# Optimization experiments

Hardware: AMD Instinct MI355X
Metric: run time of the kernel (lower is better)

Reference implementation:

```python
import jax, jax.numpy as jnp
import numpy as np

N, E = 50000, 800000
D_IN, D_HID, D_OUT, K = 128, 64, 64, 3
SLOPE = 0.2


def _xavier(key, shape):
    fan_out, fan_in = shape[0], shape[-1]
    if len(shape) == 3:  # att param (1, heads, 2*out)
        fan_out, fan_in = shape[1], shape[2]
    a = jnp.sqrt(6.0 / (fan_in + fan_out)).astype(jnp.float32)
    return jax.random.uniform(key, shape, jnp.float32, -a, a)


def setup_inputs() -> dict:
    key = jax.random.key(0)
    ks = jax.random.split(key, 9)
    x = jax.random.normal(ks[0], (N, D_IN), jnp.float32)
    edge_index = jax.random.randint(ks[1], (2, E), 0, N, jnp.int64)
    return {
        "x": x,
        "edge_index": edge_index,
        "W1": _xavier(ks[2], (D_HID, D_IN)),        # lin weight layer 1
        "att1": _xavier(ks[3], (1, 1, 2 * D_HID)),
        "bias1": jnp.zeros((D_HID,), jnp.float32),
        "resW1": _xavier(ks[4], (D_HID, D_IN)),     # res_fc (128 != 64)
        "W2": _xavier(ks[5], (D_OUT, D_HID)),       # lin weight layer 2
        "att2": _xavier(ks[6], (1, 1, 2 * D_OUT)),
        "bias2": jnp.zeros((D_OUT,), jnp.float32),
    }


def _agdn_conv(x, src, dst, W, att, bias, resW, heads):
    n = x.shape[0]
    h0 = (x @ W.T).reshape(n, heads, -1)                      # [N, h, out]
    feats = [h0]
    f = h0
    for _ in range(K):  # K-hop scatter-add propagation
        f = jax.ops.segment_sum(f[src], dst, num_segments=n)  # [N, h, out]
        feats.append(f)
    stack = jnp.stack(feats, axis=2)                          # [N, h, K+1, out]
    cat = jnp.concatenate(
        [jnp.broadcast_to(h0[:, :, None, :], stack.shape), stack], axis=-1
    )                                                         # [N, h, K+1, 2*out]
    score = jax.nn.leaky_relu((cat * att).sum(-1), SLOPE)     # [N, h, K+1]
    attn = jax.nn.softmax(score, axis=2)[..., None]
    out = (stack * attn).sum(axis=2).reshape(n, -1)           # [N, h*out]
    res = (x @ resW.T) if resW is not None else h0.reshape(n, -1)
    return out + res + bias


def reference(x, edge_index, W1, att1, bias1, resW1, W2, att2, bias2):
    src, dst = edge_index[0], edge_index[1]
    h = _agdn_conv(x, src, dst, W1, att1, bias1, resW1, heads=1)
    h = jax.nn.elu(h)  # eval mode: dropout is identity
    out = _agdn_conv(h, src, dst, W2, att2, bias2, None, heads=1)
    return out
```

## Files before the change

kernel.cpp:

```cpp
#include <hip/hip_runtime.h>
#include <math.h>


#define EPB 4096
#define CAP 8192

typedef __attribute__((ext_vector_type(8))) short bf16x8;
typedef __attribute__((ext_vector_type(4))) float f32x4;
typedef __attribute__((ext_vector_type(2))) float f32x2;

__device__ __forceinline__ unsigned short f2bf(float f)
{
    unsigned int t = __builtin_bit_cast(unsigned int, f);
    t += 0x7FFFu + ((t >> 16) & 1u);
    return (unsigned short)(t >> 16);
}
__device__ __forceinline__ float bflo(unsigned int u)
{
    return __builtin_bit_cast(float, u << 16);
}
__device__ __forceinline__ float bfhi(unsigned int u)
{
    return __builtin_bit_cast(float, u & 0xFFFF0000u);
}
__device__ __forceinline__ f32x2 up2v(unsigned int u)
{
    f32x2 r;
    r.x = bflo(u);
    r.y = bfhi(u);
    return r;
}

#define LD1 136
__global__ __launch_bounds__(256)
void gemm_l1_mfma(const float* __restrict__ x,
                  const unsigned short* __restrict__ w1b,
                  unsigned short* __restrict__ h0, float* __restrict__ res, int n)
{
    __shared__ unsigned short xs[64 * LD1];
    __shared__ unsigned short ws[128 * LD1];
    const int tid = threadIdx.x;
    const int n0 = blockIdx.x * 64;

    for (int i = tid; i < 128 * 16; i += 256) {
        int r = i >> 4, c8 = (i & 15) * 8;
        *(uint4*)&ws[r * LD1 + c8] = *(const uint4*)&w1b[r * 128 + c8];
    }
    for (int i = tid; i < 64 * 32; i += 256) {
        int r = i >> 5, c4 = (i & 31) * 4;
        int nn = n0 + r;
        float4 v = (nn < n) ? *(const float4*)&x[(size_t)nn * 128 + c4]
                            : make_float4(0.f, 0.f, 0.f, 0.f);
        uint2 o;
        o.x = (unsigned)f2bf(v.x) | ((unsigned)f2bf(v.y) << 16);
        o.y = (unsigned)f2bf(v.z) | ((unsigned)f2bf(v.w) << 16);
        *(uint2*)&xs[r * LD1 + c4] = o;
    }
    __syncthreads();

    const int wv = tid >> 6, l = tid & 63;
    const int lrow = l & 15, lk = l >> 4;
    f32x4 acc[8] = {};
    const unsigned short* ax = &xs[(wv * 16 + lrow) * LD1 + lk * 8];
    const unsigned short* bw = &ws[lrow * LD1 + lk * 8];

    #pragma unroll
    for (int s = 0; s < 4; ++s) {
        bf16x8 a = *(const bf16x8*)&ax[s * 32];
        #pragma unroll
        for (int t = 0; t < 8; ++t) {
            bf16x8 b = *(const bf16x8*)&bw[(size_t)t * 16 * LD1 + s * 32];
            acc[t] = __builtin_amdgcn_mfma_f32_16x16x32_bf16(a, b, acc[t], 0, 0, 0);
        }
    }

    #pragma unroll
    for (int t = 0; t < 8; ++t) {
        #pragma unroll
        for (int r = 0; r < 4; ++r) {
            int node = n0 + wv * 16 + lk * 4 + r;
            if (node < n) {
                if (t < 4) h0[(size_t)node * 64 + t * 16 + lrow] = f2bf(acc[t][r]);
                else       res[(size_t)node * 64 + (t - 4) * 16 + lrow] = acc[t][r];
            }
        }
    }
}

#define LD2 72
__global__ __launch_bounds__(256)
void gemm_l2_mfma(const float* __restrict__ h,
                  const unsigned short* __restrict__ w2b,
                  unsigned short* __restrict__ h0, int n)
{
    __shared__ unsigned short xs[64 * LD2];
    __shared__ unsigned short ws[64 * LD2];
    const int tid = threadIdx.x;
    const int n0 = blockIdx.x * 64;

    for (int i = tid; i < 64 * 8; i += 256) {
        int r = i >> 3, c8 = (i & 7) * 8;
        *(uint4*)&ws[r * LD2 + c8] = *(const uint4*)&w2b[r * 64 + c8];
    }
    for (int i = tid; i < 64 * 16; i += 256) {
        int r = i >> 4, c4 = (i & 15) * 4;
        int nn = n0 + r;
        float4 v = (nn < n) ? *(const float4*)&h[(size_t)nn * 64 + c4]
                            : make_float4(0.f, 0.f, 0.f, 0.f);
        uint2 o;
        o.x = (unsigned)f2bf(v.x) | ((unsigned)f2bf(v.y) << 16);
        o.y = (unsigned)f2bf(v.z) | ((unsigned)f2bf(v.w) << 16);
        *(uint2*)&xs[r * LD2 + c4] = o;
    }
    __syncthreads();

    const int wv = tid >> 6, l = tid & 63;
    const int lrow = l & 15, lk = l >> 4;
    f32x4 acc[4] = {};
    const unsigned short* ax = &xs[(wv * 16 + lrow) * LD2 + lk * 8];
    const unsigned short* bw = &ws[lrow * LD2 + lk * 8];

    #pragma unroll
    for (int s = 0; s < 2; ++s) {
        bf16x8 a = *(const bf16x8*)&ax[s * 32];
        #pragma unroll
        for (int t = 0; t < 4; ++t) {
            bf16x8 b = *(const bf16x8*)&bw[(size_t)t * 16 * LD2 + s * 32];
            acc[t] = __builtin_amdgcn_mfma_f32_16x16x32_bf16(a, b, acc[t], 0, 0, 0);
        }
    }

    #pragma unroll
    for (int t = 0; t < 4; ++t) {
        #pragma unroll
        for (int r = 0; r < 4; ++r) {
            int node = n0 + wv * 16 + lk * 4 + r;
            if (node < n)
                h0[(size_t)node * 64 + t * 16 + lrow] = f2bf(acc[t][r]);
        }
    }
}

__global__ __launch_bounds__(256)
void part_hist_kernel(const int* __restrict__ dst, int* __restrict__ table,
                      int E, int NB,
                      const float* __restrict__ W1, const float* __restrict__ Wres,
                      const float* __restrict__ W2,
                      unsigned short* __restrict__ w1b, unsigned short* __restrict__ w2b)
{
    int gi = blockIdx.x * 256 + threadIdx.x;
    if (gi < 8192)       w1b[gi] = f2bf(W1[gi]);
    else if (gi < 16384) w1b[gi] = f2bf(Wres[gi - 8192]);
    else if (gi < 20480) w2b[gi - 16384] = f2bf(W2[gi - 16384]);

    __shared__ int h[256];
    h[threadIdx.x] = 0;
    __syncthreads();
    int base = blockIdx.x * EPB;
    for (int i = threadIdx.x; i < EPB; i += 256) {
        int e = base + i;
        if (e < E) atomicAdd(&h[((unsigned)dst[e]) >> 8], 1);
    }
    __syncthreads();
    table[threadIdx.x * NB + blockIdx.x] = h[threadIdx.x];
}

__global__ __launch_bounds__(256)
void scanA_kernel(const int* __restrict__ cnt, int* __restrict__ excl,
                  int* __restrict__ bsum, int n)
{
    __shared__ int sh[256];
    int i = blockIdx.x * 256 + threadIdx.x;
    int v = (i < n) ? cnt[i] : 0;
    sh[threadIdx.x] = v;
    __syncthreads();
    #pragma unroll
    for (int off = 1; off < 256; off <<= 1) {
        int t = (threadIdx.x >= off) ? sh[threadIdx.x - off] : 0;
        __syncthreads();
        sh[threadIdx.x] += t;
        __syncthreads();
    }
    if (i < n) excl[i] = sh[threadIdx.x] - v;
    if (threadIdx.x == 255) bsum[blockIdx.x] = sh[255];
}

__global__ __launch_bounds__(256)
void part_scatter_kernel(const int* __restrict__ src, const int* __restrict__ dst,
                         const int* __restrict__ exclT, const int* __restrict__ bsumT,
                         unsigned int* __restrict__ packed, int E, int NB, int nbT)
{
    __shared__ int lhist[256];
    __shared__ int sh[256];
    __shared__ int lexcl[256];
    __shared__ int lcur[256];
    __shared__ int gb2[256];
    __shared__ int bofsL[256];
    __shared__ unsigned int lp[EPB];
    __shared__ unsigned char lbin[EPB];

    const int tid = threadIdx.x;
    const int base = blockIdx.x * EPB;
    const int cntE = min(EPB, E - base);

    unsigned int pv[16];
    int pb[16];
    lhist[tid] = 0;
    __syncthreads();
    #pragma unroll
    for (int it = 0; it < 16; ++it) {
        int i = it * 256 + tid;
        pv[it] = 0; pb[it] = -1;
        if (i < cntE) {
            int e = base + i;
            unsigned int p = (((unsigned)dst[e]) << 16) | (unsigned)src[e];
            pv[it] = p;
            pb[it] = (int)(p >> 24);
            atomicAdd(&lhist[pb[it]], 1);
        }
    }
    __syncthreads();
    sh[tid] = lhist[tid];
    __syncthreads();
    #pragma unroll
    for (int off = 1; off < 256; off <<= 1) {
        int t = (tid >= off) ? sh[tid - off] : 0;
        __syncthreads();
        sh[tid] += t;
        __syncthreads();
    }
    lexcl[tid] = sh[tid] - lhist[tid];
    lcur[tid] = sh[tid] - lhist[tid];
    __syncthreads();
    int bv = (tid < nbT) ? bsumT[tid] : 0;
    sh[tid] = bv;
    __syncthreads();
    #pragma unroll
    for (int off = 1; off < 256; off <<= 1) {
        int t = (tid >= off) ? sh[tid - off] : 0;
        __syncthreads();
        sh[tid] += t;
        __syncthreads();
    }
    bofsL[tid] = sh[tid] - bv;
    __syncthreads();
    int ti = tid * NB + blockIdx.x;
    gb2[tid] = exclT[ti] + bofsL[ti >> 8] - lexcl[tid];
    __syncthreads();
    #pragma unroll
    for (int it = 0; it < 16; ++it) {
        if (pb[it] >= 0) {
            int slot = atomicAdd(&lcur[pb[it]], 1);
            lp[slot] = pv[it];
            lbin[slot] = (unsigned char)pb[it];
        }
    }
    __syncthreads();
    for (int i = tid; i < cntE; i += 256)
        packed[gb2[lbin[i]] + i] = lp[i];
}

__global__ __launch_bounds__(256)
void bucket_build_kernel(const unsigned int* __restrict__ packed,
                         const int* __restrict__ exclT, const int* __restrict__ bsumT,
                         int* __restrict__ rowptr, int* __restrict__ col,
                         int E, int NB, int N, int nbT)
{
    __shared__ int h[256];
    __shared__ int sh[256];
    __shared__ int lcur[256];
    __shared__ int bofsL[256];
    __shared__ unsigned int lp[CAP];
    __shared__ unsigned short colS[CAP];

    const int b = blockIdx.x;
    const int t = threadIdx.x;

    int bv = (t < nbT) ? bsumT[t] : 0;
    sh[t] = bv;
    __syncthreads();
    #pragma unroll
    for (int off = 1; off < 256; off <<= 1) {
        int v = (t >= off) ? sh[t - off] : 0;
        __syncthreads();
        sh[t] += v;
        __syncthreads();
    }
    bofsL[t] = sh[t] - bv;
    __syncthreads();

    int i0 = exclT[b * NB] + bofsL[(b * NB) >> 8];
    int bn = (b + 1) * NB;
    int i1 = (b == gridDim.x - 1) ? E : (exclT[bn] + bofsL[bn >> 8]);
    int cB = i1 - i0;

    h[t] = 0;
    __syncthreads();
    for (int i = t; i < cB; i += 256) {
        unsigned int p = packed[i0 + i];
        if (i < CAP) lp[i] = p;
        atomicAdd(&h[(p >> 16) & 255], 1);
    }
    __syncthreads();
    sh[t] = h[t];
    __syncthreads();
    #pragma unroll
    for (int off = 1; off < 256; off <<= 1) {
        int v = (t >= off) ? sh[t - off] : 0;
        __syncthreads();
        sh[t] += v;
        __syncthreads();
    }
    int excl = sh[t] - h[t];
    int d = b * 256 + t;
    if (d < N) rowptr[d] = i0 + excl;
    if (b == gridDim.x - 1 && t == 0) rowptr[N] = E;
    lcur[t] = excl;
    __syncthreads();
    for (int i = t; i < cB; i += 256) {
        unsigned int p = (i < CAP) ? lp[i] : packed[i0 + i];
        int lo = (p >> 16) & 255;
        int r = atomicAdd(&lcur[lo], 1);
        if (r < CAP) colS[r] = (unsigned short)(p & 0xFFFFu);
        else col[i0 + r] = (int)(p & 0xFFFFu);
    }
    __syncthreads();
    for (int i = t; i < cB && i < CAP; i += 256)
        col[i0 + i] = (int)colS[i];
}

__global__ __launch_bounds__(256)
void hop_csr_kernel(const unsigned short* __restrict__ fin,
                    unsigned short* __restrict__ fout,
                    const int* __restrict__ rowptr, const int* __restrict__ col, int n)
{
    int lane = threadIdx.x & 63;
    int node = blockIdx.x * 8 + ((threadIdx.x >> 6) << 1) + (lane >> 5);
    if (node >= n) return;
    int sub = (lane >> 3) & 3;
    int fo = (lane & 7) * 8;

    int beg = rowptr[node], end = rowptr[node + 1];
    f32x2 ac[4] = {};
    for (int b = beg + sub; b < end; b += 16) {
        int e1 = b + 4, e2 = b + 8, e3 = b + 12;
        uint4 u0 = *(const uint4*)&fin[(size_t)col[b] * 64 + fo];
        uint4 u1 = make_uint4(0, 0, 0, 0);
        uint4 u2 = make_uint4(0, 0, 0, 0);
        uint4 u3 = make_uint4(0, 0, 0, 0);
        if (e1 < end) u1 = *(const uint4*)&fin[(size_t)col[e1] * 64 + fo];
        if (e2 < end) u2 = *(const uint4*)&fin[(size_t)col[e2] * 64 + fo];
        if (e3 < end) u3 = *(const uint4*)&fin[(size_t)col[e3] * 64 + fo];
        ac[0] += up2v(u0.x); ac[1] += up2v(u0.y);
        ac[2] += up2v(u0.z); ac[3] += up2v(u0.w);
        ac[0] += up2v(u1.x); ac[1] += up2v(u1.y);
        ac[2] += up2v(u1.z); ac[3] += up2v(u1.w);
        ac[0] += up2v(u2.x); ac[1] += up2v(u2.y);
        ac[2] += up2v(u2.z); ac[3] += up2v(u2.w);
        ac[0] += up2v(u3.x); ac[1] += up2v(u3.y);
        ac[2] += up2v(u3.z); ac[3] += up2v(u3.w);
    }
    float a[8] = {ac[0].x, ac[0].y, ac[1].x, ac[1].y,
                  ac[2].x, ac[2].y, ac[3].x, ac[3].y};
    #pragma unroll
    for (int off = 8; off <= 16; off <<= 1)
        #pragma unroll
        for (int k = 0; k < 8; ++k)
            a[k] += __shfl_xor(a[k], off);
    if (sub == 0) {
        uint4 o;
        o.x = (unsigned)f2bf(a[0]) | ((unsigned)f2bf(a[1]) << 16);
        o.y = (unsigned)f2bf(a[2]) | ((unsigned)f2bf(a[3]) << 16);
        o.z = (unsigned)f2bf(a[4]) | ((unsigned)f2bf(a[5]) << 16);
        o.w = (unsigned)f2bf(a[6]) | ((unsigned)f2bf(a[7]) << 16);
        *(uint4*)&fout[(size_t)node * 64 + fo] = o;
    }
}

template<int MODE>
__global__ __launch_bounds__(256)
void hop3_combine_kernel(const unsigned short* __restrict__ h0,
                         const unsigned short* __restrict__ f1,
                         const unsigned short* __restrict__ f2,
                         const float* __restrict__ res, const float* __restrict__ att,
                         const float* __restrict__ bias, float* __restrict__ out,
                         const int* __restrict__ rowptr, const int* __restrict__ col, int n)
{
    int lane = threadIdx.x & 63;
    int node = blockIdx.x * 8 + ((threadIdx.x >> 6) << 1) + (lane >> 5);
    if (node >= n) return;
    int sub = (lane >> 3) & 3;
    int fo = (lane & 7) * 8;
    size_t rbase = (size_t)node * 64 + fo;

    int beg = rowptr[node], end = rowptr[node + 1];
    f32x2 ac[4] = {};
    for (int b = beg + sub; b < end; b += 16) {
        int e1 = b + 4, e2 = b + 8, e3 = b + 12;
        uint4 u0 = *(const uint4*)&f2[(size_t)col[b] * 64 + fo];
        uint4 u1 = make_uint4(0, 0, 0, 0);
        uint4 u2 = make_uint4(0, 0, 0, 0);
        uint4 u3 = make_uint4(0, 0, 0, 0);
        if (e1 < end) u1 = *(const uint4*)&f2[(size_t)col[e1] * 64 + fo];
        if (e2 < end) u2 = *(const uint4*)&f2[(size_t)col[e2] * 64 + fo];
        if (e3 < end) u3 = *(const uint4*)&f2[(size_t)col[e3] * 64 + fo];
        ac[0] += up2v(u0.x); ac[1] += up2v(u0.y);
        ac[2] += up2v(u0.z); ac[3] += up2v(u0.w);
        ac[0] += up2v(u1.x); ac[1] += up2v(u1.y);
        ac[2] += up2v(u1.z); ac[3] += up2v(u1.w);
        ac[0] += up2v(u2.x); ac[1] += up2v(u2.y);
        ac[2] += up2v(u2.z); ac[3] += up2v(u2.w);
        ac[0] += up2v(u3.x); ac[1] += up2v(u3.y);
        ac[2] += up2v(u3.z); ac[3] += up2v(u3.w);
    }
    float a[8] = {ac[0].x, ac[0].y, ac[1].x, ac[1].y,
                  ac[2].x, ac[2].y, ac[3].x, ac[3].y};
    #pragma unroll
    for (int off = 8; off <= 16; off <<= 1)
        #pragma unroll
        for (int k = 0; k < 8; ++k)
            a[k] += __shfl_xor(a[k], off);

    uint4 r0 = *(const uint4*)&h0[rbase];
    uint4 r1 = *(const uint4*)&f1[rbase];
    uint4 r2 = *(const uint4*)&f2[rbase];
    float v0f[8] = {bflo(r0.x), bfhi(r0.x), bflo(r0.y), bfhi(r0.y),
                    bflo(r0.z), bfhi(r0.z), bflo(r0.w), bfhi(r0.w)};
    float v1f[8] = {bflo(r1.x), bfhi(r1.x), bflo(r1.y), bfhi(r1.y),
                    bflo(r1.z), bfhi(r1.z), bflo(r1.w), bfhi(r1.w)};
    float v2f[8] = {bflo(r2.x), bfhi(r2.x), bflo(r2.y), bfhi(r2.y),
                    bflo(r2.z), bfhi(r2.z), bflo(r2.w), bfhi(r2.w)};

    float4 alo0 = *(const float4*)&att[fo];
    float4 alo1 = *(const float4*)&att[fo + 4];
    float4 ahi0 = *(const float4*)&att[64 + fo];
    float4 ahi1 = *(const float4*)&att[64 + fo + 4];
    float alo[8] = {alo0.x, alo0.y, alo0.z, alo0.w, alo1.x, alo1.y, alo1.z, alo1.w};
    float ahi[8] = {ahi0.x, ahi0.y, ahi0.z, ahi0.w, ahi1.x, ahi1.y, ahi1.z, ahi1.w};

    float p0 = 0.f, q0 = 0.f, q1 = 0.f, q2 = 0.f, q3 = 0.f;
    #pragma unroll
    for (int j = 0; j < 8; ++j) {
        p0 += v0f[j] * alo[j];
        q0 += v0f[j] * ahi[j];
        q1 += v1f[j] * ahi[j];
        q2 += v2f[j] * ahi[j];
        q3 += a[j]   * ahi[j];
    }
    #pragma unroll
    for (int off = 1; off <= 4; off <<= 1) {
        p0 += __shfl_xor(p0, off);
        q0 += __shfl_xor(q0, off);
        q1 += __shfl_xor(q1, off);
        q2 += __shfl_xor(q2, off);
        q3 += __shfl_xor(q3, off);
    }

    float s0 = p0 + q0, s1 = p0 + q1, s2 = p0 + q2, s3 = p0 + q3;
    s0 = s0 > 0.f ? s0 : 0.2f * s0;
    s1 = s1 > 0.f ? s1 : 0.2f * s1;
    s2 = s2 > 0.f ? s2 : 0.2f * s2;
    s3 = s3 > 0.f ? s3 : 0.2f * s3;
    float m = fmaxf(fmaxf(s0, s1), fmaxf(s2, s3));
    float E0 = __expf(s0 - m), E1 = __expf(s1 - m);
    float E2 = __expf(s2 - m), E3 = __expf(s3 - m);
    float inv = 1.f / (E0 + E1 + E2 + E3);
    float w0 = E0 * inv, w1 = E1 * inv, w2 = E2 * inv, w3 = E3 * inv;

    float rsv[8];
    if (MODE == 0) {
        float4 ra = *(const float4*)&res[rbase];
        float4 rb = *(const float4*)&res[rbase + 4];
        rsv[0] = ra.x; rsv[1] = ra.y; rsv[2] = ra.z; rsv[3] = ra.w;
        rsv[4] = rb.x; rsv[5] = rb.y; rsv[6] = rb.z; rsv[7] = rb.w;
    } else {
        #pragma unroll
        for (int j = 0; j < 8; ++j) rsv[j] = v0f[j];
    }
    float4 ba = *(const float4*)&bias[fo];
    float4 bb = *(const float4*)&bias[fo + 4];
    float bi[8] = {ba.x, ba.y, ba.z, ba.w, bb.x, bb.y, bb.z, bb.w};

    float o[8];
    #pragma unroll
    for (int j = 0; j < 8; ++j) {
        float v = w0 * v0f[j] + w1 * v1f[j] + w2 * v2f[j] + w3 * a[j];
        v += rsv[j] + bi[j];
        if (MODE == 0) v = v > 0.f ? v : __expf(v) - 1.f;
        o[j] = v;
    }
    if (sub == 0) {
        *(float4*)&out[rbase]     = make_float4(o[0], o[1], o[2], o[3]);
        *(float4*)&out[rbase + 4] = make_float4(o[4], o[5], o[6], o[7]);
    }
}

extern "C" void kernel_launch(void* const* d_in, const int* in_sizes, int n_in,
                              void* d_out, int out_size, void* d_ws, size_t ws_size,
                              hipStream_t stream)
{
    const float* x     = (const float*)d_in[0];
    const int*   ei    = (const int*)  d_in[1];
    const float* W1    = (const float*)d_in[2];
    const float* att1  = (const float*)d_in[3];
    const float* bias1 = (const float*)d_in[4];
    const float* resW1 = (const float*)d_in[5];
    const float* W2    = (const float*)d_in[6];
    const float* att2  = (const float*)d_in[7];
    const float* bias2 = (const float*)d_in[8];

    const int N_ = in_sizes[0] / 128;
    const int E_ = in_sizes[1] / 2;
    const int* src = ei;
    const int* dst = ei + E_;

    float* out = (float*)d_out;
    size_t S = (size_t)N_ * 64;
    unsigned short* h0 = (unsigned short*)d_ws;
    unsigned short* f1 = h0 + S;
    unsigned short* f2 = f1 + S;
    int* rowptr = (int*)(f2 + S);
    int* col    = rowptr + (N_ + 1);

    const int NB    = (E_ + EPB - 1) / EPB;
    const int NBUCK = (N_ + 255) / 256;

    unsigned int* packed = (unsigned int*)f1;
    int* table = (int*)(col + E_);
    int* exclT = table + 256 * NB;
    int* bsumT = exclT + 256 * NB;
    unsigned short* w1b = (unsigned short*)(bsumT + 256);
    unsigned short* w2b = w1b + 16384;

    dim3 blk(256);
    int grid_g    = (N_ + 63) / 64;
    int node_grid = (N_ + 7) / 8;
    int nT        = 256 * NB;
    int nbT       = (nT + 255) / 256;

    part_hist_kernel<<<NB, blk, 0, stream>>>(dst, table, E_, NB,
                                             W1, resW1, W2, w1b, w2b);
    scanA_kernel<<<nbT, blk, 0, stream>>>(table, exclT, bsumT, nT);
    part_scatter_kernel<<<NB, blk, 0, stream>>>(src, dst, exclT, bsumT, packed,
                                                E_, NB, nbT);
    bucket_build_kernel<<<NBUCK, blk, 0, stream>>>(packed, exclT, bsumT, rowptr, col,
                                                   E_, NB, N_, nbT);

    gemm_l1_mfma<<<grid_g, blk, 0, stream>>>(x, w1b, h0, out, N_);
    hop_csr_kernel<<<node_grid, blk, 0, stream>>>(h0, f1, rowptr, col, N_);
    hop_csr_kernel<<<node_grid, blk, 0, stream>>>(f1, f2, rowptr, col, N_);
    hop3_combine_kernel<0><<<node_grid, blk, 0, stream>>>(h0, f1, f2, out, att1, bias1, out,
                                                          rowptr, col, N_);

    gemm_l2_mfma<<<grid_g, blk, 0, stream>>>(out, w2b, h0, N_);
    hop_csr_kernel<<<node_grid, blk, 0, stream>>>(h0, f1, rowptr, col, N_);
    hop_csr_kernel<<<node_grid, blk, 0, stream>>>(f1, f2, rowptr, col, N_);
    hop3_combine_kernel<1><<<node_grid, blk, 0, stream>>>(h0, f1, f2, nullptr, att2, bias2, out,
                                                          rowptr, col, N_);
}
```

Before: 177.4 us.

## Fuse layer-1 GEMM with edge histogram kernel and drop bin byte array

The edge-partition histogram and the layer-1 MFMA GEMM now run as one launch, with the first NB blocks doing histogram work and the rest doing the GEMM. Each GEMM block converts W1/Wres from fp32 to bf16 itself instead of reading a prepacked buffer. This removes one kernel launch and lets the two independent stages overlap on the GPU. The scatter kernel also drops its lbin shared array and recomputes the bin from the packed word's top byte. In exchange, every GEMM block repeats the weight conversion.

```diff
diff --git a/kernel.cpp b/kernel.cpp
--- a/kernel.cpp
+++ b/kernel.cpp
@@ -33,18 +33,46 @@
 
 #define LD1 136
 __global__ __launch_bounds__(256)
-void gemm_l1_mfma(const float* __restrict__ x,
-                  const unsigned short* __restrict__ w1b,
-                  unsigned short* __restrict__ h0, float* __restrict__ res, int n)
+void gemm_l1_hist_kernel(const float* __restrict__ x,
+                         const float* __restrict__ W1, const float* __restrict__ Wres,
+                         unsigned short* __restrict__ h0, float* __restrict__ res, int n,
+                         const int* __restrict__ dst, int* __restrict__ table,
+                         int E, int NB,
+                         const float* __restrict__ W2, unsigned short* __restrict__ w2b)
 {
     __shared__ unsigned short xs[64 * LD1];
     __shared__ unsigned short ws[128 * LD1];
     const int tid = threadIdx.x;
-    const int n0 = blockIdx.x * 64;
-
-    for (int i = tid; i < 128 * 16; i += 256) {
-        int r = i >> 4, c8 = (i & 15) * 8;
-        *(uint4*)&ws[r * LD1 + c8] = *(const uint4*)&w1b[r * 128 + c8];
+
+    if ((int)blockIdx.x < NB) {
+        int hb = blockIdx.x;
+        int gi = hb * 256 + tid;
+        if (gi < 4096) w2b[gi] = f2bf(W2[gi]);
+
+        int* h = (int*)xs;
+        h[tid] = 0;
+        __syncthreads();
+        int base = hb * EPB;
+        for (int i = tid; i < EPB; i += 256) {
+            int e = base + i;
+            if (e < E) atomicAdd(&h[((unsigned)dst[e]) >> 8], 1);
+        }
+        __syncthreads();
+        table[tid * NB + hb] = h[tid];
+        return;
+    }
+
+    const int n0 = ((int)blockIdx.x - NB) * 64;
+
+    for (int i = tid; i < 128 * 32; i += 256) {
+        int r = i >> 5, c4 = (i & 31) * 4;
+        const float* wsrc = (r < 64) ? &W1[(size_t)r * 128 + c4]
+                                     : &Wres[(size_t)(r - 64) * 128 + c4];
+        float4 v = *(const float4*)wsrc;
+        uint2 o;
+        o.x = (unsigned)f2bf(v.x) | ((unsigned)f2bf(v.y) << 16);
+        o.y = (unsigned)f2bf(v.z) | ((unsigned)f2bf(v.w) << 16);
+        *(uint2*)&ws[r * LD1 + c4] = o;
     }
     for (int i = tid; i < 64 * 32; i += 256) {
         int r = i >> 5, c4 = (i & 31) * 4;
@@ -142,30 +170,6 @@
 }
 
 __global__ __launch_bounds__(256)
-void part_hist_kernel(const int* __restrict__ dst, int* __restrict__ table,
-                      int E, int NB,
-                      const float* __restrict__ W1, const float* __restrict__ Wres,
-                      const float* __restrict__ W2,
-                      unsigned short* __restrict__ w1b, unsigned short* __restrict__ w2b)
-{
-    int gi = blockIdx.x * 256 + threadIdx.x;
-    if (gi < 8192)       w1b[gi] = f2bf(W1[gi]);
-    else if (gi < 16384) w1b[gi] = f2bf(Wres[gi - 8192]);
-    else if (gi < 20480) w2b[gi - 16384] = f2bf(W2[gi - 16384]);
-
-    __shared__ int h[256];
-    h[threadIdx.x] = 0;
-    __syncthreads();
-    int base = blockIdx.x * EPB;
-    for (int i = threadIdx.x; i < EPB; i += 256) {
-        int e = base + i;
-        if (e < E) atomicAdd(&h[((unsigned)dst[e]) >> 8], 1);
-    }
-    __syncthreads();
-    table[threadIdx.x * NB + blockIdx.x] = h[threadIdx.x];
-}
-
-__global__ __launch_bounds__(256)
 void scanA_kernel(const int* __restrict__ cnt, int* __restrict__ excl,
                   int* __restrict__ bsum, int n)
 {
@@ -197,7 +201,6 @@
     __shared__ int gb2[256];
     __shared__ int bofsL[256];
     __shared__ unsigned int lp[EPB];
-    __shared__ unsigned char lbin[EPB];
 
     const int tid = threadIdx.x;
     const int base = blockIdx.x * EPB;
@@ -252,12 +255,13 @@
         if (pb[it] >= 0) {
             int slot = atomicAdd(&lcur[pb[it]], 1);
             lp[slot] = pv[it];
-            lbin[slot] = (unsigned char)pb[it];
-        }
-    }
-    __syncthreads();
-    for (int i = tid; i < cntE; i += 256)
-        packed[gb2[lbin[i]] + i] = lp[i];
+        }
+    }
+    __syncthreads();
+    for (int i = tid; i < cntE; i += 256) {
+        unsigned int p = lp[i];
+        packed[gb2[p >> 24] + i] = p;
+    }
 }
 
 __global__ __launch_bounds__(256)
@@ -529,8 +533,7 @@
     int* table = (int*)(col + E_);
     int* exclT = table + 256 * NB;
     int* bsumT = exclT + 256 * NB;
-    unsigned short* w1b = (unsigned short*)(bsumT + 256);
-    unsigned short* w2b = w1b + 16384;
+    unsigned short* w2b = (unsigned short*)(bsumT + 256);
 
     dim3 blk(256);
     int grid_g    = (N_ + 63) / 64;
@@ -538,15 +541,14 @@
     int nT        = 256 * NB;
     int nbT       = (nT + 255) / 256;
 
-    part_hist_kernel<<<NB, blk, 0, stream>>>(dst, table, E_, NB,
-                                             W1, resW1, W2, w1b, w2b);
+    gemm_l1_hist_kernel<<<NB + grid_g, blk, 0, stream>>>(x, W1, resW1, h0, out, N_,
+                                                         dst, table, E_, NB, W2, w2b);
     scanA_kernel<<<nbT, blk, 0, stream>>>(table, exclT, bsumT, nT);
     part_scatter_kernel<<<NB, blk, 0, stream>>>(src, dst, exclT, bsumT, packed,
                                                 E_, NB, nbT);
     bucket_build_kernel<<<NBUCK, blk, 0, stream>>>(packed, exclT, bsumT, rowptr, col,
                                                    E_, NB, N_, nbT);
 
-    gemm_l1_mfma<<<grid_g, blk, 0, stream>>>(x, w1b, h0, out, N_);
     hop_csr_kernel<<<node_grid, blk, 0, stream>>>(h0, f1, rowptr, col, N_);
     hop_csr_kernel<<<node_grid, blk, 0, stream>>>(f1, f2, rowptr, col, N_);
     hop3_combine_kernel<0><<<node_grid, blk, 0, stream>>>(h0, f1, f2, out, att1, bias1, out,
```

Measured after the change: 173.1 us. -2.4%, faster.
